# Performance work log

Measured on AMD Instinct MI355X. Metric: run time of the kernel, lower is better.

The kernel has to match this reference:

```python
import jax, jax.numpy as jnp
import numpy as np

N_NODES = 30000
N_EDGES = 480000
N_GRAPHS = 64
IN_DIM = 128
HID = 64
NEG_SLOPE = 0.2  # PyG GATConv default leaky_relu slope


def setup_inputs() -> dict:
    key = jax.random.key(0)
    ks = jax.random.split(key, 16)
    x = jax.random.normal(ks[0], (N_NODES, IN_DIM), dtype=jnp.float32)
    src = jax.random.randint(ks[1], (N_EDGES,), 0, N_NODES, dtype=jnp.int32)
    dst = jax.random.randint(ks[2], (N_EDGES,), 0, N_NODES, dtype=jnp.int32)
    edge_index = jnp.stack([src, dst], axis=0)
    # evenly-sized sorted graph assignment so every graph id is populated
    batch = (jnp.arange(N_NODES, dtype=jnp.int32) * N_GRAPHS) // N_NODES
    sc1 = 1.0 / np.sqrt(IN_DIM)
    sc2 = 1.0 / np.sqrt(4 * HID)
    sc3 = 1.0 / np.sqrt(HID)
    return dict(
        x=x, edge_index=edge_index, batch=batch,
        W1=jax.random.normal(ks[3], (IN_DIM, 4 * HID), jnp.float32) * sc1,
        att_src1=jax.random.normal(ks[4], (4, HID), jnp.float32) * sc3,
        att_dst1=jax.random.normal(ks[5], (4, HID), jnp.float32) * sc3,
        b1=jnp.zeros((4 * HID,), jnp.float32),
        W2=jax.random.normal(ks[6], (4 * HID, HID), jnp.float32) * sc2,
        att_src2=jax.random.normal(ks[7], (1, HID), jnp.float32) * sc3,
        att_dst2=jax.random.normal(ks[8], (1, HID), jnp.float32) * sc3,
        b2=jnp.zeros((HID,), jnp.float32),
        w_fc1=jax.random.normal(ks[9], (HID, HID), jnp.float32) * sc3,
        b_fc1=jnp.zeros((HID,), jnp.float32),
        w_fc2=jax.random.normal(ks[10], (HID, 2), jnp.float32) * sc3,
        b_fc2=jnp.zeros((2,), jnp.float32),
    )


def _leaky_relu(v):
    return jnp.where(v > 0, v, NEG_SLOPE * v)


def _gat_conv(x, src, dst, W, att_src, att_dst, bias, heads, ch):
    n = x.shape[0]
    h = (x @ W).reshape(n, heads, ch)                      # [N,H,C]
    a_src = jnp.sum(h * att_src[None], axis=-1)            # [N,H]
    a_dst = jnp.sum(h * att_dst[None], axis=-1)            # [N,H]
    e = _leaky_relu(a_src[src] + a_dst[dst])               # [E,H]
    e_max = jax.ops.segment_max(e, dst, num_segments=n)
    e = jnp.exp(e - e_max[dst])
    denom = jax.ops.segment_sum(e, dst, num_segments=n)
    alpha = e / denom[dst]                                 # [E,H]
    msg = h[src] * alpha[:, :, None]                       # [E,H,C]
    out = jax.ops.segment_sum(msg, dst, num_segments=n)    # [N,H,C]
    return out.reshape(n, heads * ch) + bias


def reference(x, edge_index, batch, W1, att_src1, att_dst1, b1,
              W2, att_src2, att_dst2, b2, w_fc1, b_fc1, w_fc2, b_fc2):
    n = x.shape[0]
    # add self-loops (PyG GATConv default)
    loops = jnp.arange(n, dtype=edge_index.dtype)
    src = jnp.concatenate([edge_index[0], loops])
    dst = jnp.concatenate([edge_index[1], loops])
    h = jax.nn.relu(_gat_conv(x, src, dst, W1, att_src1, att_dst1, b1, 4, HID))
    h = jax.nn.relu(_gat_conv(h, src, dst, W2, att_src2, att_dst2, b2, 1, HID))
    g = jax.ops.segment_max(h, batch, num_segments=N_GRAPHS)  # global_max_pool [G,HID]
    g = jax.nn.relu(g @ w_fc1 + b_fc1)
    logits = g @ w_fc2 + b_fc2
    return jax.nn.log_softmax(logits, axis=1)
```

## Files before the change

### kernel.cpp

```cpp
#include <hip/hip_runtime.h>
#include <hip/hip_bf16.h>
#include <math.h>

#define N_NODES  30000
#define N_EDGESR 480000
#define E_TOT    (N_EDGESR + N_NODES)
#define N_GRAPHS 64
#define IN_DIM   128
#define HID      64
#define NEG_SLOPE 0.2f

typedef __attribute__((ext_vector_type(8))) short bf16x8;
typedef __attribute__((ext_vector_type(8))) unsigned short u16x8;
typedef __attribute__((ext_vector_type(4))) float f32x4;

__device__ __forceinline__ float lrelu(float v) { return v > 0.f ? v : NEG_SLOPE * v; }
__device__ __forceinline__ float bf2f(unsigned short u) { return __uint_as_float((unsigned)u << 16); }
__device__ __forceinline__ unsigned short f2bf(float f) {
    return __bfloat16_as_ushort(__float2bfloat16(f));
}

__global__ __launch_bounds__(256) void prep_kernel(const float* __restrict__ x,
                                                   const float* __restrict__ W1,
                                                   const float* __restrict__ W2,
                                                   unsigned short* __restrict__ xb,
                                                   unsigned short* __restrict__ w1t,
                                                   unsigned short* __restrict__ w2t,
                                                   int* __restrict__ counts,
                                                   unsigned* __restrict__ g) {
    int t = blockIdx.x * 256 + threadIdx.x;
    if (t < 480000) {
        int i = t * 8;
        float4 v0 = *reinterpret_cast<const float4*>(x + i);
        float4 v1 = *reinterpret_cast<const float4*>(x + i + 4);
        u16x8 o;
        o[0] = f2bf(v0.x); o[1] = f2bf(v0.y); o[2] = f2bf(v0.z); o[3] = f2bf(v0.w);
        o[4] = f2bf(v1.x); o[5] = f2bf(v1.y); o[6] = f2bf(v1.z); o[7] = f2bf(v1.w);
        *reinterpret_cast<u16x8*>(xb + i) = o;
    } else if (t < 510000) {
        counts[t - 480000] = 0;
    } else if (t < 514096) {
        g[t - 510000] = 0u;
    } else if (t < 546864) {
        int id = t - 514096;
        int k = id >> 8, n = id & 255;
        w1t[n * 128 + k] = f2bf(W1[id]);
    } else if (t < 563248) {
        int id = t - 546864;
        int k = id >> 6, n = id & 63;
        w2t[n * 256 + k] = f2bf(W2[id]);
    }
}

__global__ void edge_hist(const int* __restrict__ ei, int* __restrict__ counts) {
    int e = blockIdx.x * blockDim.x + threadIdx.x;
    if (e >= E_TOT) return;
    int d = (e < N_EDGESR) ? ei[N_EDGESR + e] : (e - N_EDGESR);
    atomicAdd(&counts[d], 1);
}

__global__ __launch_bounds__(1024) void scan_counts(const int* __restrict__ counts,
                                                    int* __restrict__ rowstart,
                                                    int* __restrict__ cursor) {
    __shared__ int bufA[1024];
    __shared__ int bufB[1024];
    const int t = threadIdx.x;
    const int CH = 30;
    int local[CH];
    int base = t * CH;
    int s = 0;
    #pragma unroll
    for (int i = 0; i < CH; ++i) {
        int idx = base + i;
        int c = (idx < N_NODES) ? counts[idx] : 0;
        local[i] = c; s += c;
    }
    bufA[t] = s;
    __syncthreads();
    int* a = bufA; int* b = bufB;
    for (int off = 1; off < 1024; off <<= 1) {
        int v = a[t] + ((t >= off) ? a[t - off] : 0);
        b[t] = v;
        __syncthreads();
        int* tmp = a; a = b; b = tmp;
    }
    int run = (t == 0) ? 0 : a[t - 1];
    #pragma unroll
    for (int i = 0; i < CH; ++i) {
        int idx = base + i;
        if (idx < N_NODES) { rowstart[idx] = run; cursor[idx] = run; run += local[i]; }
    }
    if (t == 0) rowstart[N_NODES] = E_TOT;
}

__global__ void edge_scatter(const int* __restrict__ ei, int* __restrict__ cursor,
                             int* __restrict__ srcidx) {
    int e = blockIdx.x * blockDim.x + threadIdx.x;
    if (e >= E_TOT) return;
    int s, d;
    if (e < N_EDGESR) { s = ei[e]; d = ei[N_EDGESR + e]; }
    else              { s = d = e - N_EDGESR; }
    int pos = atomicAdd(&cursor[d], 1);
    srcidx[pos] = s;
}

__global__ __launch_bounds__(256) void mfma_gemm1(const unsigned short* __restrict__ xb,
                                                  const unsigned short* __restrict__ w1t,
                                                  unsigned short* __restrict__ h1,
                                                  const float* __restrict__ att_src,
                                                  const float* __restrict__ att_dst,
                                                  float* __restrict__ a_src,
                                                  float* __restrict__ a_dst) {
    __shared__ __align__(16) unsigned short As[64 * 128];
    const int tid = threadIdx.x;
    const int w = tid >> 6;
    const int l = tid & 63;
    const int rowbase = blockIdx.x * 64;
    char* Ab = (char*)As;

    #pragma unroll
    for (int i = 0; i < 4; ++i) {
        int flat = i * 256 + tid;
        int r = flat >> 4;
        int cb = (flat & 15) * 16;
        int gr = rowbase + r; if (gr >= N_NODES) gr = N_NODES - 1;
        int4 v = *reinterpret_cast<const int4*>(xb + (size_t)gr * 128 + (cb >> 1));
        *reinterpret_cast<int4*>(Ab + r * 256 + (cb ^ ((r & 7) << 4))) = v;
    }
    __syncthreads();

    const int lm = l & 15, lh = l >> 4;
    f32x4 acc[4][4];
    #pragma unroll
    for (int rt = 0; rt < 4; ++rt)
        #pragma unroll
        for (int ct = 0; ct < 4; ++ct)
            acc[rt][ct] = (f32x4){0.f, 0.f, 0.f, 0.f};

    #pragma unroll
    for (int s = 0; s < 4; ++s) {
        bf16x8 bfr[4], afr[4];
        #pragma unroll
        for (int ct = 0; ct < 4; ++ct) {
            int n = w * 64 + ct * 16 + lm;
            bfr[ct] = *reinterpret_cast<const bf16x8*>(w1t + n * 128 + s * 32 + lh * 8);
        }
        #pragma unroll
        for (int rt = 0; rt < 4; ++rt) {
            int row = rt * 16 + lm;
            int cb = s * 64 + lh * 16;
            afr[rt] = *reinterpret_cast<const bf16x8*>(Ab + row * 256 + (cb ^ ((row & 7) << 4)));
        }
        #pragma unroll
        for (int rt = 0; rt < 4; ++rt)
            #pragma unroll
            for (int ct = 0; ct < 4; ++ct)
                acc[rt][ct] = __builtin_amdgcn_mfma_f32_16x16x32_bf16(bfr[ct], afr[rt], acc[rt][ct], 0, 0, 0);
    }

    #pragma unroll
    for (int rt = 0; rt < 4; ++rt) {
        int row = rowbase + rt * 16 + lm;
        float ps = 0.f, pd = 0.f;
        #pragma unroll
        for (int ct = 0; ct < 4; ++ct) {
            int col = w * 64 + ct * 16 + lh * 4;
            if (row < N_NODES) {
                ushort4 o;
                o.x = f2bf(acc[rt][ct][0]); o.y = f2bf(acc[rt][ct][1]);
                o.z = f2bf(acc[rt][ct][2]); o.w = f2bf(acc[rt][ct][3]);
                *reinterpret_cast<ushort4*>(h1 + (size_t)row * 256 + col) = o;
            }
            #pragma unroll
            for (int q = 0; q < 4; ++q) {
                ps += acc[rt][ct][q] * att_src[col + q];
                pd += acc[rt][ct][q] * att_dst[col + q];
            }
        }
        ps += __shfl_xor(ps, 16); ps += __shfl_xor(ps, 32);
        pd += __shfl_xor(pd, 16); pd += __shfl_xor(pd, 32);
        if (lh == 0 && row < N_NODES) {
            a_src[row * 4 + w] = ps;
            a_dst[row * 4 + w] = pd;
        }
    }
}

__global__ __launch_bounds__(256) void gat_agg1(const unsigned short* __restrict__ h1,
                                                const float* __restrict__ a_src,
                                                const float* __restrict__ a_dst,
                                                const int* __restrict__ rowstart,
                                                const int* __restrict__ srcidx,
                                                const float* __restrict__ b1,
                                                unsigned short* __restrict__ out1) {
    int n = (blockIdx.x * 256 + threadIdx.x) >> 6;
    int lane = threadIdx.x & 63;
    if (n >= N_NODES) return;
    int beg = rowstart[n], end = rowstart[n + 1];
    const int h    = lane & 3;
    const int slot = lane >> 2;
    const int half = lane >> 5;
    const int cl   = lane & 31;
    const int myhead = cl >> 3;
    float ad_h = a_dst[n * 4 + h];

    float acc[8] = {};
    float den_part = 0.f;
    int cb = beg;
    for (; cb + 16 <= end; cb += 16) {
        int s = srcidx[cb + slot];
        float w = __expf(lrelu(a_src[s * 4 + h] + ad_h));
        den_part += w;
        #pragma unroll
        for (int j = 0; j < 16; j += 2) {
            int e = j + half;
            float wj = __shfl(w, e * 4 + myhead);
            int   sj = __shfl(s, e * 4);
            u16x8 hv = *reinterpret_cast<const u16x8*>(h1 + (size_t)sj * 256 + cl * 8);
            #pragma unroll
            for (int q = 0; q < 8; ++q) acc[q] += wj * bf2f((unsigned short)hv[q]);
        }
    }
    if (cb < end) {
        int cnt = end - cb;
        float w = 0.f; int s = 0;
        if (slot < cnt) {
            s = srcidx[cb + slot];
            w = __expf(lrelu(a_src[s * 4 + h] + ad_h));
            den_part += w;
        }
        for (int j = 0; j < cnt; j += 2) {
            int e = j + half;
            float wj = __shfl(w, e * 4 + myhead);
            int   sj = __shfl(s, e * 4);
            if (e < cnt) {
                u16x8 hv = *reinterpret_cast<const u16x8*>(h1 + (size_t)sj * 256 + cl * 8);
                #pragma unroll
                for (int q = 0; q < 8; ++q) acc[q] += wj * bf2f((unsigned short)hv[q]);
            }
        }
    }
    #pragma unroll
    for (int q = 0; q < 8; ++q) acc[q] += __shfl_xor(acc[q], 32);
    #pragma unroll
    for (int off = 4; off < 64; off <<= 1) den_part += __shfl_xor(den_part, off);
    float inv = 1.f / __shfl(den_part, myhead);
    if (half == 0) {
        float4 bv0 = *reinterpret_cast<const float4*>(b1 + cl * 8);
        float4 bv1 = *reinterpret_cast<const float4*>(b1 + cl * 8 + 4);
        u16x8 o;
        o[0] = f2bf(fmaxf(acc[0] * inv + bv0.x, 0.f));
        o[1] = f2bf(fmaxf(acc[1] * inv + bv0.y, 0.f));
        o[2] = f2bf(fmaxf(acc[2] * inv + bv0.z, 0.f));
        o[3] = f2bf(fmaxf(acc[3] * inv + bv0.w, 0.f));
        o[4] = f2bf(fmaxf(acc[4] * inv + bv1.x, 0.f));
        o[5] = f2bf(fmaxf(acc[5] * inv + bv1.y, 0.f));
        o[6] = f2bf(fmaxf(acc[6] * inv + bv1.z, 0.f));
        o[7] = f2bf(fmaxf(acc[7] * inv + bv1.w, 0.f));
        *reinterpret_cast<u16x8*>(out1 + (size_t)n * 256 + cl * 8) = o;
    }
}

__global__ __launch_bounds__(256) void mfma_gemm2(const unsigned short* __restrict__ a1b,
                                                  const unsigned short* __restrict__ w2t,
                                                  unsigned short* __restrict__ h2,
                                                  const float* __restrict__ att_src,
                                                  const float* __restrict__ att_dst,
                                                  float* __restrict__ a_src,
                                                  float* __restrict__ a_dst) {
    __shared__ __align__(16) unsigned short As[64 * 256];
    __shared__ float ps_s[4][64], pd_s[4][64];
    const int tid = threadIdx.x;
    const int w = tid >> 6, l = tid & 63;
    const int rowbase = blockIdx.x * 64;
    char* Ab = (char*)As;

    #pragma unroll
    for (int i = 0; i < 8; ++i) {
        int flat = i * 256 + tid;
        int r = flat >> 5;
        int cb = (flat & 31) * 16;
        int gr = rowbase + r; if (gr >= N_NODES) gr = N_NODES - 1;
        int4 v = *reinterpret_cast<const int4*>(a1b + (size_t)gr * 256 + (cb >> 1));
        *reinterpret_cast<int4*>(Ab + r * 512 + (cb ^ ((r & 7) << 4))) = v;
    }
    __syncthreads();

    const int lm = l & 15, lh = l >> 4;
    f32x4 acc[4];
    #pragma unroll
    for (int rt = 0; rt < 4; ++rt) acc[rt] = (f32x4){0.f, 0.f, 0.f, 0.f};

    #pragma unroll
    for (int s = 0; s < 8; ++s) {
        int n = w * 16 + lm;
        bf16x8 bf = *reinterpret_cast<const bf16x8*>(w2t + n * 256 + s * 32 + lh * 8);
        #pragma unroll
        for (int rt = 0; rt < 4; ++rt) {
            int row = rt * 16 + lm;
            int cb = s * 64 + lh * 16;
            bf16x8 af = *reinterpret_cast<const bf16x8*>(Ab + row * 512 + (cb ^ ((row & 7) << 4)));
            acc[rt] = __builtin_amdgcn_mfma_f32_16x16x32_bf16(bf, af, acc[rt], 0, 0, 0);
        }
    }

    #pragma unroll
    for (int rt = 0; rt < 4; ++rt) {
        int row = rowbase + rt * 16 + lm;
        int col = w * 16 + lh * 4;
        float ps = 0.f, pd = 0.f;
        if (row < N_NODES) {
            ushort4 o;
            o.x = f2bf(acc[rt][0]); o.y = f2bf(acc[rt][1]);
            o.z = f2bf(acc[rt][2]); o.w = f2bf(acc[rt][3]);
            *reinterpret_cast<ushort4*>(h2 + (size_t)row * 64 + col) = o;
        }
        #pragma unroll
        for (int q = 0; q < 4; ++q) {
            ps += acc[rt][q] * att_src[col + q];
            pd += acc[rt][q] * att_dst[col + q];
        }
        ps += __shfl_xor(ps, 16); ps += __shfl_xor(ps, 32);
        pd += __shfl_xor(pd, 16); pd += __shfl_xor(pd, 32);
        if (lh == 0) { ps_s[w][rt * 16 + lm] = ps; pd_s[w][rt * 16 + lm] = pd; }
    }
    __syncthreads();
    if (tid < 64) {
        int row = rowbase + tid;
        if (row < N_NODES) {
            a_src[row] = ps_s[0][tid] + ps_s[1][tid] + ps_s[2][tid] + ps_s[3][tid];
            a_dst[row] = pd_s[0][tid] + pd_s[1][tid] + pd_s[2][tid] + pd_s[3][tid];
        }
    }
}

__global__ __launch_bounds__(256) void gat_agg2_pool(const unsigned short* __restrict__ h2,
                                                     const float* __restrict__ a_src,
                                                     const float* __restrict__ a_dst,
                                                     const int* __restrict__ rowstart,
                                                     const int* __restrict__ srcidx,
                                                     const float* __restrict__ b2,
                                                     const int* __restrict__ batch,
                                                     unsigned* __restrict__ g) {
    __shared__ float sm[4][64];
    const int wid = threadIdx.x >> 6;
    const int lane = threadIdx.x & 63;
    const int n = blockIdx.x * 4 + wid;
    const int grp = lane >> 4;
    const int cl  = lane & 15;
    int beg = rowstart[n], end = rowstart[n + 1];
    float ad = a_dst[n];

    float4 acc = make_float4(0.f, 0.f, 0.f, 0.f);
    float den_part = 0.f;
    int cb = beg;
    for (; cb + 16 <= end; cb += 16) {
        float w = 0.f; int s = 0;
        if (lane < 16) {
            s = srcidx[cb + lane];
            w = __expf(lrelu(a_src[s] + ad));
            den_part += w;
        }
        #pragma unroll
        for (int j = 0; j < 16; j += 4) {
            float wj = __shfl(w, j + grp);
            int   sj = __shfl(s, j + grp);
            ushort4 hv = *reinterpret_cast<const ushort4*>(&h2[(size_t)sj * 64 + cl * 4]);
            acc.x += wj * bf2f(hv.x); acc.y += wj * bf2f(hv.y);
            acc.z += wj * bf2f(hv.z); acc.w += wj * bf2f(hv.w);
        }
    }
    if (cb < end) {
        int cnt = end - cb;
        float w = 0.f; int s = 0;
        if (lane < cnt) {
            s = srcidx[cb + lane];
            w = __expf(lrelu(a_src[s] + ad));
            den_part += w;
        }
        for (int j = 0; j < cnt; j += 4) {
            float wj = __shfl(w, j + grp);
            int   sj = __shfl(s, j + grp);
            if (j + grp < cnt) {
                ushort4 hv = *reinterpret_cast<const ushort4*>(&h2[(size_t)sj * 64 + cl * 4]);
                acc.x += wj * bf2f(hv.x); acc.y += wj * bf2f(hv.y);
                acc.z += wj * bf2f(hv.z); acc.w += wj * bf2f(hv.w);
            }
        }
    }
    #pragma unroll
    for (int off = 16; off < 64; off <<= 1) {
        acc.x += __shfl_xor(acc.x, off);
        acc.y += __shfl_xor(acc.y, off);
        acc.z += __shfl_xor(acc.z, off);
        acc.w += __shfl_xor(acc.w, off);
    }
    #pragma unroll
    for (int off = 1; off < 64; off <<= 1) den_part += __shfl_xor(den_part, off);
    float inv = 1.f / den_part;
    float4 bv = *reinterpret_cast<const float4*>(&b2[cl * 4]);
    if (lane < 16) {
        float4 val;
        val.x = fmaxf(acc.x * inv + bv.x, 0.f);
        val.y = fmaxf(acc.y * inv + bv.y, 0.f);
        val.z = fmaxf(acc.z * inv + bv.z, 0.f);
        val.w = fmaxf(acc.w * inv + bv.w, 0.f);
        *reinterpret_cast<float4*>(&sm[wid][cl * 4]) = val;
    }
    __syncthreads();
    int b0 = batch[blockIdx.x * 4];
    int b3 = batch[blockIdx.x * 4 + 3];
    if (b0 == b3) {
        if (threadIdx.x < 64) {
            float v = fmaxf(fmaxf(sm[0][threadIdx.x], sm[1][threadIdx.x]),
                            fmaxf(sm[2][threadIdx.x], sm[3][threadIdx.x]));
            atomicMax(&g[b0 * 64 + threadIdx.x], __float_as_uint(v));
        }
    } else {
        if (lane < 16) {
            int bb = batch[n];
            #pragma unroll
            for (int k = 0; k < 4; ++k)
                atomicMax(&g[bb * 64 + cl * 4 + k], __float_as_uint(sm[wid][cl * 4 + k]));
        }
    }
}

__global__ __launch_bounds__(256) void head_kernel(const float* __restrict__ g,
                                                   const float* __restrict__ w_fc1,
                                                   const float* __restrict__ b_fc1,
                                                   const float* __restrict__ w_fc2,
                                                   const float* __restrict__ b_fc2,
                                                   float* __restrict__ out) {
    __shared__ float gs[64][65];
    __shared__ float hs[64][65];
    int t = threadIdx.x;
    #pragma unroll
    for (int it = 0; it < 16; ++it) {
        int flat = it * 256 + t;
        gs[flat >> 6][flat & 63] = g[flat];
    }
    __syncthreads();
    #pragma unroll
    for (int it = 0; it < 16; ++it) {
        int flat = it * 256 + t;
        int i = flat >> 6, j = flat & 63;
        float s = b_fc1[j];
        #pragma unroll 8
        for (int k = 0; k < 64; ++k) s += gs[i][k] * w_fc1[k * 64 + j];
        hs[i][j] = fmaxf(s, 0.f);
    }
    __syncthreads();
    if (t < 64) {
        float l0 = b_fc2[0], l1 = b_fc2[1];
        #pragma unroll 8
        for (int k = 0; k < 64; ++k) {
            float v = hs[t][k];
            l0 += v * w_fc2[k * 2];
            l1 += v * w_fc2[k * 2 + 1];
        }
        float mx = fmaxf(l0, l1);
        float lse = mx + logf(__expf(l0 - mx) + __expf(l1 - mx));
        out[t * 2]     = l0 - lse;
        out[t * 2 + 1] = l1 - lse;
    }
}

extern "C" void kernel_launch(void* const* d_in, const int* in_sizes, int n_in,
                              void* d_out, int out_size, void* d_ws, size_t ws_size,
                              hipStream_t stream) {
    const float* x        = (const float*)d_in[0];
    const int*   ei       = (const int*)d_in[1];
    const int*   batch    = (const int*)d_in[2];
    const float* W1       = (const float*)d_in[3];
    const float* att_src1 = (const float*)d_in[4];
    const float* att_dst1 = (const float*)d_in[5];
    const float* b1       = (const float*)d_in[6];
    const float* W2       = (const float*)d_in[7];
    const float* att_src2 = (const float*)d_in[8];
    const float* att_dst2 = (const float*)d_in[9];
    const float* b2       = (const float*)d_in[10];
    const float* w_fc1    = (const float*)d_in[11];
    const float* b_fc1    = (const float*)d_in[12];
    const float* w_fc2    = (const float*)d_in[13];
    const float* b_fc2    = (const float*)d_in[14];

    char* ws = (char*)d_ws;
    size_t off = 0;
    auto alloc = [&](size_t bytes) -> char* {
        char* p = ws + off;
        off += (bytes + 255) & ~(size_t)255;
        return p;
    };
    unsigned short* xb   = (unsigned short*)alloc((size_t)N_NODES * 128 * 2);
    unsigned short* w1t  = (unsigned short*)alloc((size_t)256 * 128 * 2);
    unsigned short* w2t  = (unsigned short*)alloc((size_t)64 * 256 * 2);
    unsigned short* h1   = (unsigned short*)alloc((size_t)N_NODES * 256 * 2);
    unsigned short* out1 = (unsigned short*)alloc((size_t)N_NODES * 256 * 2);
    unsigned short* h2   = (unsigned short*)alloc((size_t)N_NODES * 64 * 2);
    float*    as1        = (float*)alloc((size_t)N_NODES * 4 * 4);
    float*    ad1        = (float*)alloc((size_t)N_NODES * 4 * 4);
    float*    as2        = (float*)alloc((size_t)N_NODES * 4);
    float*    ad2        = (float*)alloc((size_t)N_NODES * 4);
    int*      counts     = (int*)alloc((size_t)N_NODES * 4);
    int*      rowstart   = (int*)alloc((size_t)(N_NODES + 4) * 4);
    int*      cursor     = (int*)alloc((size_t)(N_NODES + 4) * 4);
    int*      srcidx     = (int*)alloc((size_t)E_TOT * 4);
    unsigned* g          = (unsigned*)alloc((size_t)N_GRAPHS * HID * 4);

    prep_kernel<<<2201, 256, 0, stream>>>(x, W1, W2, xb, w1t, w2t, counts, g);
    edge_hist<<<(E_TOT + 255) / 256, 256, 0, stream>>>(ei, counts);
    scan_counts<<<1, 1024, 0, stream>>>(counts, rowstart, cursor);
    edge_scatter<<<(E_TOT + 255) / 256, 256, 0, stream>>>(ei, cursor, srcidx);
    mfma_gemm1<<<(N_NODES + 63) / 64, 256, 0, stream>>>(xb, w1t, h1, att_src1, att_dst1, as1, ad1);
    gat_agg1<<<7500, 256, 0, stream>>>(h1, as1, ad1, rowstart, srcidx, b1, out1);
    mfma_gemm2<<<(N_NODES + 63) / 64, 256, 0, stream>>>(out1, w2t, h2, att_src2, att_dst2, as2, ad2);
    gat_agg2_pool<<<7500, 256, 0, stream>>>(h2, as2, ad2, rowstart, srcidx, b2, batch, g);
    head_kernel<<<1, 256, 0, stream>>>((const float*)g, w_fc1, b_fc1, w_fc2, b_fc2, (float*)d_out);
}
```

Baseline: 191.3 us.

## Degree-sort nodes for aggregation and fuse scatter, ordering and GEMM1 launches

A degree histogram is built in the scan kernel and used to compute a node order bucketed by in-degree. Both aggregation kernels then process nodes in that order, so each block's waves have similar edge counts. The edge scatter, node ordering and first GEMM are merged into one launch using block-index ranges, which removes two kernel launches. Pooling now does a per-node atomicMax instead of a shared-memory block reduction. The degree ordering loses locality between consecutive nodes, raises atomic traffic on the pooled output, and makes the node order nondeterministic.

```diff
diff --git a/kernel.cpp b/kernel.cpp
--- a/kernel.cpp
+++ b/kernel.cpp
@@ -61,9 +61,11 @@
 
 __global__ __launch_bounds__(1024) void scan_counts(const int* __restrict__ counts,
                                                     int* __restrict__ rowstart,
-                                                    int* __restrict__ cursor) {
+                                                    int* __restrict__ cursor,
+                                                    int* __restrict__ bucketcur) {
     __shared__ int bufA[1024];
     __shared__ int bufB[1024];
+    __shared__ int hist[64];
     const int t = threadIdx.x;
     const int CH = 30;
     int local[CH];
@@ -76,6 +78,7 @@
         local[i] = c; s += c;
     }
     bufA[t] = s;
+    if (t < 64) hist[t] = 0;
     __syncthreads();
     int* a = bufA; int* b = bufB;
     for (int off = 1; off < 1024; off <<= 1) {
@@ -88,34 +91,60 @@
     #pragma unroll
     for (int i = 0; i < CH; ++i) {
         int idx = base + i;
-        if (idx < N_NODES) { rowstart[idx] = run; cursor[idx] = run; run += local[i]; }
+        if (idx < N_NODES) {
+            rowstart[idx] = run; cursor[idx] = run; run += local[i];
+            atomicAdd(&hist[min(local[i], 63)], 1);
+        }
     }
     if (t == 0) rowstart[N_NODES] = E_TOT;
-}
-
-__global__ void edge_scatter(const int* __restrict__ ei, int* __restrict__ cursor,
-                             int* __restrict__ srcidx) {
-    int e = blockIdx.x * blockDim.x + threadIdx.x;
-    if (e >= E_TOT) return;
-    int s, d;
-    if (e < N_EDGESR) { s = ei[e]; d = ei[N_EDGESR + e]; }
-    else              { s = d = e - N_EDGESR; }
-    int pos = atomicAdd(&cursor[d], 1);
-    srcidx[pos] = s;
-}
-
-__global__ __launch_bounds__(256) void mfma_gemm1(const unsigned short* __restrict__ xb,
-                                                  const unsigned short* __restrict__ w1t,
-                                                  unsigned short* __restrict__ h1,
-                                                  const float* __restrict__ att_src,
-                                                  const float* __restrict__ att_dst,
-                                                  float* __restrict__ a_src,
-                                                  float* __restrict__ a_dst) {
+    __syncthreads();
+    if (t == 0) {
+        int racc = 0;
+        for (int d = 0; d < 64; ++d) { bucketcur[d] = racc; racc += hist[d]; }
+    }
+}
+
+#define SCAT_B 1993
+#define ORD_B  118
+#define G1_B   469
+__global__ __launch_bounds__(256) void scatter_order_gemm1(const int* __restrict__ ei,
+                                                           int* __restrict__ cursor,
+                                                           int* __restrict__ srcidx,
+                                                           const int* __restrict__ rowstart,
+                                                           int* __restrict__ bucketcur,
+                                                           int* __restrict__ nodeorder,
+                                                           const unsigned short* __restrict__ xb,
+                                                           const unsigned short* __restrict__ w1t,
+                                                           unsigned short* __restrict__ h1,
+                                                           const float* __restrict__ att_src,
+                                                           const float* __restrict__ att_dst,
+                                                           float* __restrict__ a_src,
+                                                           float* __restrict__ a_dst) {
     __shared__ __align__(16) unsigned short As[64 * 128];
+    const int b = blockIdx.x;
     const int tid = threadIdx.x;
+    if (b < SCAT_B) {
+        int e = b * 256 + tid;
+        if (e >= E_TOT) return;
+        int s, d;
+        if (e < N_EDGESR) { s = ei[e]; d = ei[N_EDGESR + e]; }
+        else              { s = d = e - N_EDGESR; }
+        int pos = atomicAdd(&cursor[d], 1);
+        srcidx[pos] = s;
+        return;
+    }
+    if (b < SCAT_B + ORD_B) {
+        int n = (b - SCAT_B) * 256 + tid;
+        if (n < N_NODES) {
+            int deg = rowstart[n + 1] - rowstart[n];
+            int pos = atomicAdd(&bucketcur[min(deg, 63)], 1);
+            nodeorder[pos] = n;
+        }
+        return;
+    }
     const int w = tid >> 6;
     const int l = tid & 63;
-    const int rowbase = blockIdx.x * 64;
+    const int rowbase = (b - SCAT_B - ORD_B) * 64;
     char* Ab = (char*)As;
 
     #pragma unroll
@@ -191,11 +220,12 @@
                                                 const float* __restrict__ a_dst,
                                                 const int* __restrict__ rowstart,
                                                 const int* __restrict__ srcidx,
+                                                const int* __restrict__ nodeorder,
                                                 const float* __restrict__ b1,
                                                 unsigned short* __restrict__ out1) {
-    int n = (blockIdx.x * 256 + threadIdx.x) >> 6;
+    int widx = (blockIdx.x * 256 + threadIdx.x) >> 6;
     int lane = threadIdx.x & 63;
-    if (n >= N_NODES) return;
+    int n = nodeorder[widx];
     int beg = rowstart[n], end = rowstart[n + 1];
     const int h    = lane & 3;
     const int slot = lane >> 2;
@@ -339,13 +369,14 @@
                                                      const float* __restrict__ a_dst,
                                                      const int* __restrict__ rowstart,
                                                      const int* __restrict__ srcidx,
+                                                     const int* __restrict__ nodeorder,
                                                      const float* __restrict__ b2,
                                                      const int* __restrict__ batch,
                                                      unsigned* __restrict__ g) {
-    __shared__ float sm[4][64];
     const int wid = threadIdx.x >> 6;
     const int lane = threadIdx.x & 63;
-    const int n = blockIdx.x * 4 + wid;
+    const int widx = blockIdx.x * 4 + wid;
+    const int n = nodeorder[widx];
     const int grp = lane >> 4;
     const int cl  = lane & 15;
     int beg = rowstart[n], end = rowstart[n + 1];
@@ -400,29 +431,12 @@
     float inv = 1.f / den_part;
     float4 bv = *reinterpret_cast<const float4*>(&b2[cl * 4]);
     if (lane < 16) {
-        float4 val;
-        val.x = fmaxf(acc.x * inv + bv.x, 0.f);
-        val.y = fmaxf(acc.y * inv + bv.y, 0.f);
-        val.z = fmaxf(acc.z * inv + bv.z, 0.f);
-        val.w = fmaxf(acc.w * inv + bv.w, 0.f);
-        *reinterpret_cast<float4*>(&sm[wid][cl * 4]) = val;
-    }
-    __syncthreads();
-    int b0 = batch[blockIdx.x * 4];
-    int b3 = batch[blockIdx.x * 4 + 3];
-    if (b0 == b3) {
-        if (threadIdx.x < 64) {
-            float v = fmaxf(fmaxf(sm[0][threadIdx.x], sm[1][threadIdx.x]),
-                            fmaxf(sm[2][threadIdx.x], sm[3][threadIdx.x]));
-            atomicMax(&g[b0 * 64 + threadIdx.x], __float_as_uint(v));
-        }
-    } else {
-        if (lane < 16) {
-            int bb = batch[n];
-            #pragma unroll
-            for (int k = 0; k < 4; ++k)
-                atomicMax(&g[bb * 64 + cl * 4 + k], __float_as_uint(sm[wid][cl * 4 + k]));
-        }
+        int bb = batch[n];
+        unsigned* gp = g + bb * 64 + cl * 4;
+        atomicMax(gp + 0, __float_as_uint(fmaxf(acc.x * inv + bv.x, 0.f)));
+        atomicMax(gp + 1, __float_as_uint(fmaxf(acc.y * inv + bv.y, 0.f)));
+        atomicMax(gp + 2, __float_as_uint(fmaxf(acc.z * inv + bv.z, 0.f)));
+        atomicMax(gp + 3, __float_as_uint(fmaxf(acc.w * inv + bv.w, 0.f)));
     }
 }
 
@@ -506,15 +520,18 @@
     int*      rowstart   = (int*)alloc((size_t)(N_NODES + 4) * 4);
     int*      cursor     = (int*)alloc((size_t)(N_NODES + 4) * 4);
     int*      srcidx     = (int*)alloc((size_t)E_TOT * 4);
+    int*      bucketcur  = (int*)alloc((size_t)64 * 4);
+    int*      nodeorder  = (int*)alloc((size_t)N_NODES * 4);
     unsigned* g          = (unsigned*)alloc((size_t)N_GRAPHS * HID * 4);
 
     prep_kernel<<<2201, 256, 0, stream>>>(x, W1, W2, xb, w1t, w2t, counts, g);
     edge_hist<<<(E_TOT + 255) / 256, 256, 0, stream>>>(ei, counts);
-    scan_counts<<<1, 1024, 0, stream>>>(counts, rowstart, cursor);
-    edge_scatter<<<(E_TOT + 255) / 256, 256, 0, stream>>>(ei, cursor, srcidx);
-    mfma_gemm1<<<(N_NODES + 63) / 64, 256, 0, stream>>>(xb, w1t, h1, att_src1, att_dst1, as1, ad1);
-    gat_agg1<<<7500, 256, 0, stream>>>(h1, as1, ad1, rowstart, srcidx, b1, out1);
+    scan_counts<<<1, 1024, 0, stream>>>(counts, rowstart, cursor, bucketcur);
+    scatter_order_gemm1<<<SCAT_B + ORD_B + G1_B, 256, 0, stream>>>(
+        ei, cursor, srcidx, rowstart, bucketcur, nodeorder,
+        xb, w1t, h1, att_src1, att_dst1, as1, ad1);
+    gat_agg1<<<7500, 256, 0, stream>>>(h1, as1, ad1, rowstart, srcidx, nodeorder, b1, out1);
     mfma_gemm2<<<(N_NODES + 63) / 64, 256, 0, stream>>>(out1, w2t, h2, att_src2, att_dst2, as2, ad2);
-    gat_agg2_pool<<<7500, 256, 0, stream>>>(h2, as2, ad2, rowstart, srcidx, b2, batch, g);
+    gat_agg2_pool<<<7500, 256, 0, stream>>>(h2, as2, ad2, rowstart, srcidx, nodeorder, b2, batch, g);
     head_kernel<<<1, 256, 0, stream>>>((const float*)g, w_fc1, b_fc1, w_fc2, b_fc2, (float*)d_out);
 }
```

Measured after the change: 298.7 us. +56.1%, slower.
